# Kernel optimization log

Hardware: AMD Instinct MI355X
Metric: run time of the kernel (lower is better)

The kernel has to match this reference:

```python
import jax, jax.numpy as jnp
import numpy as np

B, N, H, NH = 2, 1024, 1024, 16  # batch, seq per branch, hidden, heads


def setup_inputs() -> dict:
    key = jax.random.key(0)
    k1, k2, k3, k4 = jax.random.split(key, 4)
    x = jax.random.normal(k1, (B, N, H), jnp.float32)
    x2 = jax.random.normal(k2, (B, N, H), jnp.float32)
    w_qkv = jax.random.normal(k3, (3 * H, H), jnp.float32) * 0.02  # nn.Linear(H, 3H), no bias
    w_out = jax.random.normal(k4, (H, H), jnp.float32) * 0.02
    b_out = jnp.zeros((H,), jnp.float32)
    return {"x": x, "x2": x2, "w_qkv": w_qkv, "w_out": w_out, "b_out": b_out, "num_heads": NH}


def _qkv_split(x, w_qkv, nh):
    # qkv Linear then Rearrange 'b n (qkv l d) -> qkv b l n d'
    b, n, h = x.shape
    d = h // nh
    qkv = x @ w_qkv.T                                    # [b, n, 3h]
    qkv = qkv.reshape(b, n, 3, nh, d).transpose(2, 0, 3, 1, 4)  # [3, b, nh, n, d]
    return qkv[0], qkv[1], qkv[2]


def reference(x, x2, w_qkv, w_out, b_out, num_heads):
    nh = num_heads
    d = x.shape[-1] // nh
    scale = float(d) ** -0.5
    q, k, v = _qkv_split(x, w_qkv, nh)
    q2, k2, v2 = _qkv_split(x2, w_qkv, nh)
    # cross-branch concat along seq dim
    q = jnp.concatenate([q, q2], axis=2)
    k = jnp.concatenate([k, k2], axis=2)
    v = jnp.concatenate([v, v2], axis=2)
    att = jax.nn.softmax(jnp.einsum('bhxd,bhyd->bhxy', q, k) * scale, axis=-1)  # [b,nh,2N,2N]
    o = jnp.einsum('bhxy,bhyd->bhxd', att, v)            # [b,nh,2N,d]
    o1, o2 = jnp.split(o, 2, axis=2)

    def proj(o):
        b, h, n, dd = o.shape
        o = o.transpose(0, 2, 1, 3).reshape(b, n, h * dd)  # 'b h l d -> b l (h d)'
        return o @ w_out.T + b_out

    return proj(o1), proj(o2)
```

## Files before the change

### kernel.cpp

```cpp
#include <hip/hip_runtime.h>
#include <hip/hip_bf16.h>

#define NB      2
#define NSEQ    1024
#define S2      2048
#define HDIM    1024
#define NHEADS  16
#define DHEAD   64
#define Q_SCALE 0.18033688011112042f

typedef unsigned short ushort_t;
typedef __attribute__((ext_vector_type(8))) short short8;
typedef __attribute__((ext_vector_type(4))) float f32x4;

__device__ __forceinline__ ushort_t f2bf(float f) {
    union { float f; unsigned int u; } c; c.f = f;
    unsigned int u = c.u;
    u += 0x7FFFu + ((u >> 16) & 1u);
    return (ushort_t)(u >> 16);
}

__device__ __forceinline__ unsigned pack_bf16x2(float a, float b) {
    union { __hip_bfloat162 h; unsigned u; } cv;
    cv.h = __float22bfloat162_rn(float2{a, b});
    return cv.u;
}

__global__ __launch_bounds__(256) void cvt_all(
    const float* __restrict__ x, const float* __restrict__ x2,
    const float* __restrict__ wqkv, const float* __restrict__ wout,
    ushort_t* __restrict__ Xb, ushort_t* __restrict__ Wqb, ushort_t* __restrict__ Wob)
{
    int b = blockIdx.x;
    const float* s; ushort_t* d; int i;
    if (b < 2048)      { s = x;    d = Xb;            i = b * 256 + threadIdx.x; }
    else if (b < 4096) { s = x2;   d = Xb + 2097152;  i = (b - 2048) * 256 + threadIdx.x; }
    else if (b < 7168) { s = wqkv; d = Wqb;           i = (b - 4096) * 256 + threadIdx.x; }
    else               { s = wout; d = Wob;           i = (b - 7168) * 256 + threadIdx.x; }
    float4 v = ((const float4*)s)[i];
    ushort4 o; o.x = f2bf(v.x); o.y = f2bf(v.y); o.z = f2bf(v.z); o.w = f2bf(v.w);
    ((ushort4*)d)[i] = o;
}


__global__ __launch_bounds__(256) void qkv_gemm_mfma(
    const ushort_t* __restrict__ Xb, const ushort_t* __restrict__ Wqb,
    ushort_t* __restrict__ Qb, ushort_t* __restrict__ Kb, ushort_t* __restrict__ Vtb)
{
    __shared__ ushort_t As[128 * 32];
    __shared__ ushort_t Bs[128 * 32];
    const int t = threadIdx.x;
    const int lane = t & 63, quad = lane >> 4, l15 = lane & 15;
    const int w = t >> 6;
    const int wm = (w >> 1) * 64, wn = (w & 1) * 64;
    const int r0 = blockIdx.y * 128, c0 = blockIdx.x * 128;

    const int g_chunk = (lane & 3) ^ ((lane >> 3) & 3);
    const int srow_lo = w * 16 + (lane >> 2);

    f32x4 acc[4][4];
    #pragma unroll
    for (int i = 0; i < 4; ++i)
        #pragma unroll
        for (int j = 0; j < 4; ++j) acc[i][j] = (f32x4){0.f, 0.f, 0.f, 0.f};

    for (int k0 = 0; k0 < HDIM; k0 += 32) {
        __syncthreads();
        #pragma unroll
        for (int p = 0; p < 2; ++p) {
            int row = srow_lo + p * 64;
            const ushort_t* gpA = Xb  + (size_t)(r0 + row) * HDIM + k0 + g_chunk * 8;
            const ushort_t* gpB = Wqb + (size_t)(c0 + row) * HDIM + k0 + g_chunk * 8;
            ushort_t* lpA = As + p * 2048 + w * 512;
            ushort_t* lpB = Bs + p * 2048 + w * 512;
            __builtin_amdgcn_global_load_lds(
                (const __attribute__((address_space(1))) void*)gpA,
                (__attribute__((address_space(3))) void*)lpA, 16, 0, 0);
            __builtin_amdgcn_global_load_lds(
                (const __attribute__((address_space(1))) void*)gpB,
                (__attribute__((address_space(3))) void*)lpB, 16, 0, 0);
        }
        __syncthreads();
        const int sw = (l15 >> 1) & 3;
        short8 af[4], bf[4];
        #pragma unroll
        for (int mi = 0; mi < 4; ++mi) {
            int ra = wm + mi * 16 + l15;
            af[mi] = *(const short8*)(As + ra * 32 + ((quad ^ sw) * 8));
        }
        #pragma unroll
        for (int ni = 0; ni < 4; ++ni) {
            int rb = wn + ni * 16 + l15;
            bf[ni] = *(const short8*)(Bs + rb * 32 + ((quad ^ sw) * 8));
        }
        #pragma unroll
        for (int mi = 0; mi < 4; ++mi)
            #pragma unroll
            for (int ni = 0; ni < 4; ++ni)
                acc[mi][ni] = __builtin_amdgcn_mfma_f32_16x16x32_bf16(af[mi], bf[ni], acc[mi][ni], 0, 0, 0);
    }

    const int branch = r0 >> 11;
    const int bb     = (r0 & 2047) >> 10;
    const int qi     = c0 >> 10;
    const float qsc  = (qi == 0) ? Q_SCALE : 1.0f;
    #pragma unroll
    for (int mi = 0; mi < 4; ++mi) {
        int sbase = branch * NSEQ + (r0 & 1023) + wm + mi * 16 + quad * 4;
        #pragma unroll
        for (int ni = 0; ni < 4; ++ni) {
            int cc = (c0 & 1023) + wn + ni * 16;
            int h  = cc >> 6;
            int dd = (cc & 63) + l15;
            if (qi == 2) {
                ushort4 pv;
                pv.x = f2bf(acc[mi][ni][0]); pv.y = f2bf(acc[mi][ni][1]);
                pv.z = f2bf(acc[mi][ni][2]); pv.w = f2bf(acc[mi][ni][3]);
                *(ushort4*)(Vtb + ((size_t)(bb * NHEADS + h) * DHEAD + dd) * S2 + sbase) = pv;
            } else {
                ushort_t* dst = (qi ? Kb : Qb) + ((size_t)(bb * NHEADS + h) * S2 + sbase) * DHEAD + dd;
                dst[0]   = f2bf(acc[mi][ni][0] * qsc);
                dst[64]  = f2bf(acc[mi][ni][1] * qsc);
                dst[128] = f2bf(acc[mi][ni][2] * qsc);
                dst[192] = f2bf(acc[mi][ni][3] * qsc);
            }
        }
    }
}

__global__ __launch_bounds__(256) void attn_mfma(
    const ushort_t* __restrict__ Qb, const ushort_t* __restrict__ Kb,
    const ushort_t* __restrict__ Vtb, ushort_t* __restrict__ Ob)
{
    __shared__ ushort_t Ks[2][64 * 64];
    __shared__ ushort_t Vs[2][64 * 64];
    __shared__ ushort_t Ps[64][72];

    const int t = threadIdx.x, lane = t & 63, quad = lane >> 4, l15 = lane & 15, w = t >> 6;
    const int bh = blockIdx.z * NHEADS + blockIdx.y;
    const int r0 = blockIdx.x * 64;
    const ushort_t* Qh  = Qb  + (size_t)bh * S2 * DHEAD;
    const ushort_t* Kh  = Kb  + (size_t)bh * S2 * DHEAD;
    const ushort_t* Vth = Vtb + (size_t)bh * DHEAD * S2;

    const int slot = lane & 7;
    const int rsub = lane >> 3;
    auto prefetch = [&](int kt_, int buf_) {
        #pragma unroll
        for (int c = 0; c < 2; ++c) {
            int row = w * 16 + c * 8 + rsub;
            int gK  = slot ^ ((row >> 2) & 7);
            int gV  = slot ^ (row & 7);
            const ushort_t* gpK = Kh  + (size_t)(kt_ * 64 + row) * DHEAD + gK * 8;
            const ushort_t* gpV = Vth + (size_t)row * S2 + kt_ * 64 + gV * 8;
            ushort_t* lpK = &Ks[buf_][w * 1024 + c * 512];
            ushort_t* lpV = &Vs[buf_][w * 1024 + c * 512];
            __builtin_amdgcn_global_load_lds(
                (const __attribute__((address_space(1))) void*)gpK,
                (__attribute__((address_space(3))) void*)lpK, 16, 0, 0);
            __builtin_amdgcn_global_load_lds(
                (const __attribute__((address_space(1))) void*)gpV,
                (__attribute__((address_space(3))) void*)lpV, 16, 0, 0);
        }
    };

    const int qrow = r0 + 16 * w + l15;
    short8 aq0 = *(const short8*)(Qh + (size_t)qrow * DHEAD + quad * 8);
    short8 aq1 = *(const short8*)(Qh + (size_t)qrow * DHEAD + 32 + quad * 8);

    float lacc[4] = {0.f, 0.f, 0.f, 0.f};
    f32x4 oacc[4];
    #pragma unroll
    for (int nt = 0; nt < 4; ++nt) oacc[nt] = (f32x4){0.f, 0.f, 0.f, 0.f};

    prefetch(0, 0);
    prefetch(1, 1);
    __syncthreads();

    for (int kt = 0; kt < S2 / 64; ++kt) {
        const ushort_t* kb = &Ks[kt & 1][0];
        const ushort_t* vb = &Vs[kt & 1][0];

        f32x4 sacc[4];
        #pragma unroll
        for (int nt = 0; nt < 4; ++nt) {
            const int key = 4 * l15 + nt;
            const ushort_t* krow = kb + key * 64;
            const int swz = l15 & 7;
            short8 bk0 = *(const short8*)(krow + ((quad       ^ swz) * 8));
            short8 bk1 = *(const short8*)(krow + (((4 + quad) ^ swz) * 8));
            f32x4 s = (f32x4){0.f, 0.f, 0.f, 0.f};
            s = __builtin_amdgcn_mfma_f32_16x16x32_bf16(aq0, bk0, s, 0, 0, 0);
            s = __builtin_amdgcn_mfma_f32_16x16x32_bf16(aq1, bk1, s, 0, 0, 0);
            sacc[nt] = s;
        }

        #pragma unroll
        for (int reg = 0; reg < 4; ++reg) {
            float p0 = __builtin_exp2f(sacc[0][reg]);
            float p1 = __builtin_exp2f(sacc[1][reg]);
            float p2 = __builtin_exp2f(sacc[2][reg]);
            float p3 = __builtin_exp2f(sacc[3][reg]);
            lacc[reg] += (p0 + p1) + (p2 + p3);
            uint2 pk;
            pk.x = pack_bf16x2(p0, p1);
            pk.y = pack_bf16x2(p2, p3);
            int prow = 16 * w + quad * 4 + reg;
            *(uint2*)&Ps[prow][4 * l15] = pk;
        }

        #pragma unroll
        for (int kk = 0; kk < 2; ++kk) {
            short8 pa = *(const short8*)&Ps[16 * w + l15][kk * 32 + quad * 8];
            #pragma unroll
            for (int nt = 0; nt < 4; ++nt) {
                const int drow = nt * 16 + l15;
                short8 bv = *(const short8*)(vb + drow * 64 + (((kk * 4 + quad) ^ (drow & 7)) * 8));
                oacc[nt] = __builtin_amdgcn_mfma_f32_16x16x32_bf16(pa, bv, oacc[nt], 0, 0, 0);
            }
        }

        __syncthreads();
        if (kt + 2 < S2 / 64) prefetch(kt + 2, kt & 1);
    }

    #pragma unroll
    for (int reg = 0; reg < 4; ++reg) {
        float l = lacc[reg];
        l += __shfl_xor(l, 1);
        l += __shfl_xor(l, 2);
        l += __shfl_xor(l, 4);
        l += __shfl_xor(l, 8);
        float inv = 1.f / l;
        size_t rowoff = ((size_t)bh * S2 + r0 + 16 * w + quad * 4 + reg) * DHEAD;
        #pragma unroll
        for (int nt = 0; nt < 4; ++nt)
            Ob[rowoff + nt * 16 + l15] = f2bf(oacc[nt][reg] * inv);
    }
}

__global__ __launch_bounds__(256) void proj_gemm_mfma(
    const ushort_t* __restrict__ Ob, const ushort_t* __restrict__ Wob,
    const float* __restrict__ Bo, float* __restrict__ Out)
{
    __shared__ ushort_t As[128 * 32];
    __shared__ ushort_t Bs[128 * 32];
    const int t = threadIdx.x;
    const int lane = t & 63, quad = lane >> 4, l15 = lane & 15;
    const int w = t >> 6;
    const int wm = (w >> 1) * 64, wn = (w & 1) * 64;
    const int r0 = blockIdx.y * 128, c0 = blockIdx.x * 128;
    const int branch = r0 >> 11, bb = (r0 & 2047) >> 10;

    const int g_chunk = (lane & 3) ^ ((lane >> 3) & 3);
    const int srow_lo = w * 16 + (lane >> 2);

    f32x4 acc[4][4];
    #pragma unroll
    for (int i = 0; i < 4; ++i)
        #pragma unroll
        for (int j = 0; j < 4; ++j) acc[i][j] = (f32x4){0.f, 0.f, 0.f, 0.f};

    for (int k0 = 0; k0 < HDIM; k0 += 32) {
        int h = k0 >> 6, off = k0 & 63;
        __syncthreads();
        #pragma unroll
        for (int p = 0; p < 2; ++p) {
            int row = srow_lo + p * 64;
            int s = branch * NSEQ + (r0 & 1023) + row;
            const ushort_t* gpA = Ob + ((size_t)(bb * NHEADS + h) * S2 + s) * DHEAD + off + g_chunk * 8;
            const ushort_t* gpB = Wob + (size_t)(c0 + row) * HDIM + k0 + g_chunk * 8;
            ushort_t* lpA = As + p * 2048 + w * 512;
            ushort_t* lpB = Bs + p * 2048 + w * 512;
            __builtin_amdgcn_global_load_lds(
                (const __attribute__((address_space(1))) void*)gpA,
                (__attribute__((address_space(3))) void*)lpA, 16, 0, 0);
            __builtin_amdgcn_global_load_lds(
                (const __attribute__((address_space(1))) void*)gpB,
                (__attribute__((address_space(3))) void*)lpB, 16, 0, 0);
        }
        __syncthreads();
        const int sw = (l15 >> 1) & 3;
        short8 af[4], bf[4];
        #pragma unroll
        for (int mi = 0; mi < 4; ++mi) {
            int ra = wm + mi * 16 + l15;
            af[mi] = *(const short8*)(As + ra * 32 + ((quad ^ sw) * 8));
        }
        #pragma unroll
        for (int ni = 0; ni < 4; ++ni) {
            int rb = wn + ni * 16 + l15;
            bf[ni] = *(const short8*)(Bs + rb * 32 + ((quad ^ sw) * 8));
        }
        #pragma unroll
        for (int mi = 0; mi < 4; ++mi)
            #pragma unroll
            for (int ni = 0; ni < 4; ++ni)
                acc[mi][ni] = __builtin_amdgcn_mfma_f32_16x16x32_bf16(af[mi], bf[ni], acc[mi][ni], 0, 0, 0);
    }

    #pragma unroll
    for (int mi = 0; mi < 4; ++mi) {
        int rb = r0 + wm + mi * 16 + quad * 4;
        #pragma unroll
        for (int ni = 0; ni < 4; ++ni) {
            int c = c0 + wn + ni * 16 + l15;
            float bias = Bo[c];
            Out[(size_t)(rb + 0) * HDIM + c] = acc[mi][ni][0] + bias;
            Out[(size_t)(rb + 1) * HDIM + c] = acc[mi][ni][1] + bias;
            Out[(size_t)(rb + 2) * HDIM + c] = acc[mi][ni][2] + bias;
            Out[(size_t)(rb + 3) * HDIM + c] = acc[mi][ni][3] + bias;
        }
    }
}

extern "C" void kernel_launch(void* const* d_in, const int* in_sizes, int n_in,
                              void* d_out, int out_size, void* d_ws, size_t ws_size,
                              hipStream_t stream) {
    const float* x    = (const float*)d_in[0];
    const float* x2   = (const float*)d_in[1];
    const float* wqkv = (const float*)d_in[2];
    const float* wout = (const float*)d_in[3];
    const float* bout = (const float*)d_in[4];
    float* out = (float*)d_out;

    char* ws = (char*)d_ws;
    ushort_t* Xb  = (ushort_t*)(ws);
    ushort_t* Wqb = (ushort_t*)(ws + (8u  << 20));
    ushort_t* Wob = (ushort_t*)(ws + (14u << 20));
    ushort_t* Qb  = (ushort_t*)(ws + (16u << 20));
    ushort_t* Kb  = (ushort_t*)(ws + (24u << 20));
    ushort_t* Vtb = (ushort_t*)(ws + (32u << 20));
    ushort_t* Ob  = (ushort_t*)(ws + (40u << 20));

    cvt_all<<<8192, 256, 0, stream>>>(x, x2, wqkv, wout, Xb, Wqb, Wob);
    qkv_gemm_mfma<<<dim3(24, 32), 256, 0, stream>>>(Xb, Wqb, Qb, Kb, Vtb);
    attn_mfma<<<dim3(S2 / 64, NHEADS, NB), 256, 0, stream>>>(Qb, Kb, Vtb, Ob);
    proj_gemm_mfma<<<dim3(8, 32), 256, 0, stream>>>(Ob, Wob, bout, out);
}
```

Measured before the change: 234.1 us.

## Double attention query tile per block and reuse K/V fragments across sub-tiles

```diff
diff --git a/kernel.cpp b/kernel.cpp
--- a/kernel.cpp
+++ b/kernel.cpp
@@ -41,7 +41,6 @@
     ushort4 o; o.x = f2bf(v.x); o.y = f2bf(v.y); o.z = f2bf(v.z); o.w = f2bf(v.w);
     ((ushort4*)d)[i] = o;
 }
-
 
 __global__ __launch_bounds__(256) void qkv_gemm_mfma(
     const ushort_t* __restrict__ Xb, const ushort_t* __restrict__ Wqb,
@@ -138,7 +137,7 @@
 
     const int t = threadIdx.x, lane = t & 63, quad = lane >> 4, l15 = lane & 15, w = t >> 6;
     const int bh = blockIdx.z * NHEADS + blockIdx.y;
-    const int r0 = blockIdx.x * 64;
+    const int r0 = blockIdx.x * 128;
     const ushort_t* Qh  = Qb  + (size_t)bh * S2 * DHEAD;
     const ushort_t* Kh  = Kb  + (size_t)bh * S2 * DHEAD;
     const ushort_t* Vth = Vtb + (size_t)bh * DHEAD * S2;
@@ -164,14 +163,20 @@
         }
     };
 
-    const int qrow = r0 + 16 * w + l15;
-    short8 aq0 = *(const short8*)(Qh + (size_t)qrow * DHEAD + quad * 8);
-    short8 aq1 = *(const short8*)(Qh + (size_t)qrow * DHEAD + 32 + quad * 8);
-
-    float lacc[4] = {0.f, 0.f, 0.f, 0.f};
-    f32x4 oacc[4];
-    #pragma unroll
-    for (int nt = 0; nt < 4; ++nt) oacc[nt] = (f32x4){0.f, 0.f, 0.f, 0.f};
+    short8 aq[2][2];
+    #pragma unroll
+    for (int s = 0; s < 2; ++s) {
+        const int qrow = r0 + 32 * w + 16 * s + l15;
+        aq[s][0] = *(const short8*)(Qh + (size_t)qrow * DHEAD + quad * 8);
+        aq[s][1] = *(const short8*)(Qh + (size_t)qrow * DHEAD + 32 + quad * 8);
+    }
+
+    float lacc[2][4] = {};
+    f32x4 oacc[2][4];
+    #pragma unroll
+    for (int s = 0; s < 2; ++s)
+        #pragma unroll
+        for (int nt = 0; nt < 4; ++nt) oacc[s][nt] = (f32x4){0.f, 0.f, 0.f, 0.f};
 
     prefetch(0, 0);
     prefetch(1, 1);
@@ -181,62 +186,78 @@
         const ushort_t* kb = &Ks[kt & 1][0];
         const ushort_t* vb = &Vs[kt & 1][0];
 
-        f32x4 sacc[4];
+        short8 kf[4][2];
         #pragma unroll
         for (int nt = 0; nt < 4; ++nt) {
             const int key = 4 * l15 + nt;
             const ushort_t* krow = kb + key * 64;
             const int swz = l15 & 7;
-            short8 bk0 = *(const short8*)(krow + ((quad       ^ swz) * 8));
-            short8 bk1 = *(const short8*)(krow + (((4 + quad) ^ swz) * 8));
-            f32x4 s = (f32x4){0.f, 0.f, 0.f, 0.f};
-            s = __builtin_amdgcn_mfma_f32_16x16x32_bf16(aq0, bk0, s, 0, 0, 0);
-            s = __builtin_amdgcn_mfma_f32_16x16x32_bf16(aq1, bk1, s, 0, 0, 0);
-            sacc[nt] = s;
-        }
-
+            kf[nt][0] = *(const short8*)(krow + ((quad       ^ swz) * 8));
+            kf[nt][1] = *(const short8*)(krow + (((4 + quad) ^ swz) * 8));
+        }
+
+        f32x4 sacc[2][4];
+        #pragma unroll
+        for (int s = 0; s < 2; ++s)
+            #pragma unroll
+            for (int nt = 0; nt < 4; ++nt) {
+                f32x4 sv = (f32x4){0.f, 0.f, 0.f, 0.f};
+                sv = __builtin_amdgcn_mfma_f32_16x16x32_bf16(aq[s][0], kf[nt][0], sv, 0, 0, 0);
+                sv = __builtin_amdgcn_mfma_f32_16x16x32_bf16(aq[s][1], kf[nt][1], sv, 0, 0, 0);
+                sacc[s][nt] = sv;
+            }
+
+        short8 vf[4][2];
+        #pragma unroll
+        for (int nt = 0; nt < 4; ++nt) {
+            const int drow = nt * 16 + l15;
+            vf[nt][0] = *(const short8*)(vb + drow * 64 + ((quad       ^ (drow & 7)) * 8));
+            vf[nt][1] = *(const short8*)(vb + drow * 64 + (((4 + quad) ^ (drow & 7)) * 8));
+        }
+
+        #pragma unroll
+        for (int s = 0; s < 2; ++s) {
+            #pragma unroll
+            for (int reg = 0; reg < 4; ++reg) {
+                float p0 = __builtin_exp2f(sacc[s][0][reg]);
+                float p1 = __builtin_exp2f(sacc[s][1][reg]);
+                float p2 = __builtin_exp2f(sacc[s][2][reg]);
+                float p3 = __builtin_exp2f(sacc[s][3][reg]);
+                lacc[s][reg] += (p0 + p1) + (p2 + p3);
+                uint2 pk;
+                pk.x = pack_bf16x2(p0, p1);
+                pk.y = pack_bf16x2(p2, p3);
+                int prow = 16 * w + quad * 4 + reg;
+                *(uint2*)&Ps[prow][4 * l15] = pk;
+            }
+            #pragma unroll
+            for (int kk = 0; kk < 2; ++kk) {
+                short8 pa = *(const short8*)&Ps[16 * w + l15][kk * 32 + quad * 8];
+                #pragma unroll
+                for (int nt = 0; nt < 4; ++nt)
+                    oacc[s][nt] = __builtin_amdgcn_mfma_f32_16x16x32_bf16(pa, vf[nt][kk], oacc[s][nt], 0, 0, 0);
+            }
+        }
+
+        __syncthreads();
+        if (kt + 2 < S2 / 64) prefetch(kt + 2, kt & 1);
+    }
+
+    #pragma unroll
+    for (int s = 0; s < 2; ++s)
         #pragma unroll
         for (int reg = 0; reg < 4; ++reg) {
-            float p0 = __builtin_exp2f(sacc[0][reg]);
-            float p1 = __builtin_exp2f(sacc[1][reg]);
-            float p2 = __builtin_exp2f(sacc[2][reg]);
-            float p3 = __builtin_exp2f(sacc[3][reg]);
-            lacc[reg] += (p0 + p1) + (p2 + p3);
-            uint2 pk;
-            pk.x = pack_bf16x2(p0, p1);
-            pk.y = pack_bf16x2(p2, p3);
-            int prow = 16 * w + quad * 4 + reg;
-            *(uint2*)&Ps[prow][4 * l15] = pk;
-        }
-
-        #pragma unroll
-        for (int kk = 0; kk < 2; ++kk) {
-            short8 pa = *(const short8*)&Ps[16 * w + l15][kk * 32 + quad * 8];
-            #pragma unroll
-            for (int nt = 0; nt < 4; ++nt) {
-                const int drow = nt * 16 + l15;
-                short8 bv = *(const short8*)(vb + drow * 64 + (((kk * 4 + quad) ^ (drow & 7)) * 8));
-                oacc[nt] = __builtin_amdgcn_mfma_f32_16x16x32_bf16(pa, bv, oacc[nt], 0, 0, 0);
-            }
-        }
-
-        __syncthreads();
-        if (kt + 2 < S2 / 64) prefetch(kt + 2, kt & 1);
-    }
-
-    #pragma unroll
-    for (int reg = 0; reg < 4; ++reg) {
-        float l = lacc[reg];
-        l += __shfl_xor(l, 1);
-        l += __shfl_xor(l, 2);
-        l += __shfl_xor(l, 4);
-        l += __shfl_xor(l, 8);
-        float inv = 1.f / l;
-        size_t rowoff = ((size_t)bh * S2 + r0 + 16 * w + quad * 4 + reg) * DHEAD;
-        #pragma unroll
-        for (int nt = 0; nt < 4; ++nt)
-            Ob[rowoff + nt * 16 + l15] = f2bf(oacc[nt][reg] * inv);
-    }
+            float l = lacc[s][reg];
+            l += __shfl_xor(l, 1);
+            l += __shfl_xor(l, 2);
+            l += __shfl_xor(l, 4);
+            l += __shfl_xor(l, 8);
+            float inv = 1.f / l;
+            size_t rowoff = ((size_t)bh * S2 + r0 + 32 * w + 16 * s + quad * 4 + reg) * DHEAD;
+            #pragma unroll
+            for (int nt = 0; nt < 4; ++nt)
+                Ob[rowoff + nt * 16 + l15] = f2bf(oacc[s][nt][reg] * inv);
+        }
 }
 
 __global__ __launch_bounds__(256) void proj_gemm_mfma(
@@ -335,6 +356,6 @@
 
     cvt_all<<<8192, 256, 0, stream>>>(x, x2, wqkv, wout, Xb, Wqb, Wob);
     qkv_gemm_mfma<<<dim3(24, 32), 256, 0, stream>>>(Xb, Wqb, Qb, Kb, Vtb);
-    attn_mfma<<<dim3(S2 / 64, NHEADS, NB), 256, 0, stream>>>(Qb, Kb, Vtb, Ob);
+    attn_mfma<<<dim3(S2 / 128, NHEADS, NB), 256, 0, stream>>>(Qb, Kb, Vtb, Ob);
     proj_gemm_mfma<<<dim3(8, 32), 256, 0, stream>>>(Ob, Wob, bout, out);
 }
```

Result: faster. 228.2 us (-2.5%).
